# Kernel tuning notes

Measured on AMD Instinct MI355X. Metric: run time of the kernel, lower is better.

The kernel has to match this reference:

```python
import jax, jax.numpy as jnp
import numpy as np

B, T, D, H, G = 256, 1024, 32, 64, 4 * 64  # batch, seq, input, hidden, gates


def setup_inputs() -> dict:
    key = jax.random.key(0)
    ks = jax.random.split(key, 12)
    s = 1.0 / np.sqrt(H)  # PyTorch LSTM default init scale
    return {
        "x": jax.random.normal(ks[0], (B, T, D), dtype=jnp.float32),
        "w_ih_l0": jax.random.normal(ks[1], (G, D), dtype=jnp.float32) * s,
        "w_hh_l0": jax.random.normal(ks[2], (G, H), dtype=jnp.float32) * s,
        "b_ih_l0": jax.random.normal(ks[3], (G,), dtype=jnp.float32) * s,
        "b_hh_l0": jax.random.normal(ks[4], (G,), dtype=jnp.float32) * s,
        "w_ih_l1": jax.random.normal(ks[5], (G, H), dtype=jnp.float32) * s,
        "w_hh_l1": jax.random.normal(ks[6], (G, H), dtype=jnp.float32) * s,
        "b_ih_l1": jax.random.normal(ks[7], (G,), dtype=jnp.float32) * s,
        "b_hh_l1": jax.random.normal(ks[8], (G,), dtype=jnp.float32) * s,
        "w_fc": jax.random.normal(ks[9], (1, H), dtype=jnp.float32) * s,
        "b_fc": jax.random.normal(ks[10], (1,), dtype=jnp.float32) * s,
    }


def _lstm_layer(x, w_ih, w_hh, b_ih, b_hh):
    """x: [B, T, Din] -> h_seq [B, T, H]. PyTorch gate order (i, f, g, o)."""
    # Precompute input contribution for all timesteps in one GEMM.
    gx = jnp.einsum('btd,gd->btg', x, w_ih) + b_ih + b_hh  # [B, T, 4H]
    gx = jnp.swapaxes(gx, 0, 1)  # [T, B, 4H] for scan over time
    h0 = jnp.zeros((x.shape[0], H), dtype=x.dtype)
    c0 = jnp.zeros((x.shape[0], H), dtype=x.dtype)

    def step(carry, g_t):
        h, c = carry
        g = g_t + h @ w_hh.T  # [B, 4H]
        i, f, gg, o = jnp.split(g, 4, axis=-1)
        i = jax.nn.sigmoid(i)
        f = jax.nn.sigmoid(f)
        gg = jnp.tanh(gg)
        o = jax.nn.sigmoid(o)
        c = f * c + i * gg
        h = o * jnp.tanh(c)
        return (h, c), h

    _, h_seq = jax.lax.scan(step, (h0, c0), gx)  # h_seq: [T, B, H]
    return jnp.swapaxes(h_seq, 0, 1)  # [B, T, H]


def reference(x, w_ih_l0, w_hh_l0, b_ih_l0, b_hh_l0,
              w_ih_l1, w_hh_l1, b_ih_l1, b_hh_l1, w_fc, b_fc):
    h1 = _lstm_layer(x, w_ih_l0, w_hh_l0, b_ih_l0, b_hh_l0)
    h2 = _lstm_layer(h1, w_ih_l1, w_hh_l1, b_ih_l1, b_hh_l1)
    last = h2[:, -1, :]  # [B, H]
    logits = last @ w_fc.T + b_fc  # [B, 1]
    return jax.nn.sigmoid(logits)
```

## Files before the change

kernel.cpp:

```cpp
#include <hip/hip_runtime.h>

#define TT 1024
#define DD 32
#define HH 64

typedef __fp16 h2v __attribute__((ext_vector_type(2)));
typedef _Float16 f16x8 __attribute__((ext_vector_type(8)));
typedef float f32x4 __attribute__((ext_vector_type(4)));

struct __attribute__((aligned(16))) H4 { h2v p[4]; };

__device__ __forceinline__ h2v pk(float a, float b) {
    return __builtin_amdgcn_cvt_pkrtz(a, b);
}
__device__ __forceinline__ float fsig(float x) {
    float e = __builtin_amdgcn_exp2f(-1.4426950408889634f * x);
    return __builtin_amdgcn_rcpf(1.0f + e);
}
__device__ __forceinline__ float ftanh(float x) {
    float e = __builtin_amdgcn_exp2f(2.885390081777927f * x);
    return 1.0f - 2.0f * __builtin_amdgcn_rcpf(1.0f + e);
}
__device__ __forceinline__ void bar_lds() {
    asm volatile("s_waitcnt lgkmcnt(0)\n\ts_barrier" ::: "memory");
}
__device__ __forceinline__ float pick4(f32x4 c, bool s0, bool s1) {
    float lo = s0 ? c[1] : c[0];
    float hi = s0 ? c[3] : c[2];
    return s1 ? hi : lo;
}
__device__ __forceinline__ f16x8 load_afrag(const float* p) {
    float4 f0 = *(const float4*)p;
    float4 f1 = *(const float4*)(p + 4);
    H4 t;
    t.p[0] = pk(f0.x, f0.y); t.p[1] = pk(f0.z, f0.w);
    t.p[2] = pk(f1.x, f1.y); t.p[3] = pk(f1.z, f1.w);
    return __builtin_bit_cast(f16x8, t);
}
#define MFMA16(A, B, C) __builtin_amdgcn_mfma_f32_16x16x32_f16(A, B, C, 0, 0, 0)

__global__ __launch_bounds__(512) void lstm2_b4v3(
    const float* __restrict__ x,
    const float* __restrict__ w_ih_l0, const float* __restrict__ w_hh_l0,
    const float* __restrict__ b_ih_l0, const float* __restrict__ b_hh_l0,
    const float* __restrict__ w_ih_l1, const float* __restrict__ w_hh_l1,
    const float* __restrict__ b_ih_l1, const float* __restrict__ b_hh_l1,
    const float* __restrict__ w_fc,   const float* __restrict__ b_fc,
    float* __restrict__ out)
{
    const int bbase = blockIdx.x * 4;
    const int tid  = threadIdx.x;
    const int wave = tid >> 6;
    const int lane = tid & 63;
    const bool isL1 = wave < 4;
    const int js   = wave & 3;
    const int quad = lane >> 4;
    const int bb   = lane & 3;
    const int rsel = (lane >> 2) & 3;
    const int jj   = js*16 + quad*4 + rsel;
    const int mrow = lane & 15;

    __shared__ __attribute__((aligned(16))) __fp16 buf[1280];

    {
        int* bi = (int*)buf;
        bi[tid] = 0;
        if (tid < 128) bi[512 + tid] = 0;
    }

    f16x8 A[16];
    float bs0, bs1, bs2, bs3;
    if (isL1) {
        #pragma unroll
        for (int q = 0; q < 4; ++q) {
            const int g = q*64 + js*16 + mrow;
            A[q*3 + 0] = load_afrag(w_ih_l0 + (size_t)g*DD + quad*8);
            A[q*3 + 1] = load_afrag(w_hh_l0 + (size_t)g*HH + quad*8);
            A[q*3 + 2] = load_afrag(w_hh_l0 + (size_t)g*HH + 32 + quad*8);
        }
        bs0 = b_ih_l0[0*64 + jj] + b_hh_l0[0*64 + jj];
        bs1 = b_ih_l0[1*64 + jj] + b_hh_l0[1*64 + jj];
        bs2 = b_ih_l0[2*64 + jj] + b_hh_l0[2*64 + jj];
        bs3 = b_ih_l0[3*64 + jj] + b_hh_l0[3*64 + jj];
    } else {
        #pragma unroll
        for (int q = 0; q < 4; ++q) {
            const int g = q*64 + js*16 + mrow;
            A[q*4 + 0] = load_afrag(w_ih_l1 + (size_t)g*HH + quad*8);
            A[q*4 + 1] = load_afrag(w_ih_l1 + (size_t)g*HH + 32 + quad*8);
            A[q*4 + 2] = load_afrag(w_hh_l1 + (size_t)g*HH + quad*8);
            A[q*4 + 3] = load_afrag(w_hh_l1 + (size_t)g*HH + 32 + quad*8);
        }
        bs0 = b_ih_l1[0*64 + jj] + b_hh_l1[0*64 + jj];
        bs1 = b_ih_l1[1*64 + jj] + b_hh_l1[1*64 + jj];
        bs2 = b_ih_l1[2*64 + jj] + b_hh_l1[2*64 + jj];
        bs3 = b_ih_l1[3*64 + jj] + b_hh_l1[3*64 + jj];
    }

    const int roff = (bb*4 + quad)*8;
    const int cw   = (isL1 ? 1 : 3) + (jj >> 5);
    const int woff = ((cw*4 + bb)*4 + ((jj & 31) >> 3))*8 + (jj & 7);

    const float* xg = x + (size_t)(bbase + (lane >> 4)) * (TT*DD) + (lane & 15)*2;
    const int sdw = ((lane >> 4)*4 + ((lane & 15) >> 2))*4 + ((lane & 15) & 3);
    float2 xv1 = {0.f, 0.f}, xv2 = {0.f, 0.f};

    __syncthreads();
    if (wave == 7) {
        float2 v0 = *(const float2*)xg;
        ((int*)buf)[sdw] = __builtin_bit_cast(int, pk(v0.x, v0.y));
        xv1 = *(const float2*)(xg + DD);
        xv2 = *(const float2*)(xg + 2*DD);
    }
    __syncthreads();

    const bool s0 = (rsel & 1) != 0;
    const bool s1 = (rsel & 2) != 0;
    float cst = 0.0f;

    for (int t = 0; t <= TT; ++t) {
        const int p = t & 1;
        const __fp16* bc = buf + p*640;
        __fp16* bn = buf + (p ^ 1)*640;
        if (isL1) {
            if (t < TT) {
                f16x8 B0 = *(const f16x8*)(bc + 0*128 + roff);
                f16x8 B1 = *(const f16x8*)(bc + 1*128 + roff);
                f16x8 B2 = *(const f16x8*)(bc + 2*128 + roff);

                f32x4 Z = {0.f, 0.f, 0.f, 0.f};
                f32x4 C0 = Z, C1 = Z, C2 = Z, C3 = Z;
                C0 = MFMA16(A[0], B0, C0); C0 = MFMA16(A[1],  B1, C0); C0 = MFMA16(A[2],  B2, C0);
                C1 = MFMA16(A[3], B0, C1); C1 = MFMA16(A[4],  B1, C1); C1 = MFMA16(A[5],  B2, C1);
                C2 = MFMA16(A[6], B0, C2); C2 = MFMA16(A[7],  B1, C2); C2 = MFMA16(A[8],  B2, C2);
                C3 = MFMA16(A[9], B0, C3); C3 = MFMA16(A[10], B1, C3); C3 = MFMA16(A[11], B2, C3);

                float Si = pick4(C0, s0, s1) + bs0;
                float Sf = pick4(C1, s0, s1) + bs1;
                float Sg = pick4(C2, s0, s1) + bs2;
                float So = pick4(C3, s0, s1) + bs3;

                float ii = fsig(Si), ff = fsig(Sf), oo = fsig(So);
                float gg = ftanh(Sg);
                cst = ff * cst + ii * gg;
                float hv = oo * ftanh(cst);
                bn[woff] = (__fp16)hv;
            }
        } else {
            if (wave == 7 && t < TT) {
                ((int*)bn)[sdw] = __builtin_bit_cast(int, pk(xv1.x, xv1.y));
                xv1 = xv2;
                const int tl = (t + 3 < TT) ? (t + 3) : (TT - 1);
                xv2 = *(const float2*)(xg + (size_t)tl*DD);
            }
            if (t > 0) {
                f16x8 B1 = *(const f16x8*)(bc + 1*128 + roff);
                f16x8 B2 = *(const f16x8*)(bc + 2*128 + roff);
                f16x8 B3 = *(const f16x8*)(bc + 3*128 + roff);
                f16x8 B4 = *(const f16x8*)(bc + 4*128 + roff);

                f32x4 Z = {0.f, 0.f, 0.f, 0.f};
                f32x4 C0 = Z, C1 = Z, C2 = Z, C3 = Z;
                C0 = MFMA16(A[0],  B1, C0); C0 = MFMA16(A[1],  B2, C0);
                C0 = MFMA16(A[2],  B3, C0); C0 = MFMA16(A[3],  B4, C0);
                C1 = MFMA16(A[4],  B1, C1); C1 = MFMA16(A[5],  B2, C1);
                C1 = MFMA16(A[6],  B3, C1); C1 = MFMA16(A[7],  B4, C1);
                C2 = MFMA16(A[8],  B1, C2); C2 = MFMA16(A[9],  B2, C2);
                C2 = MFMA16(A[10], B3, C2); C2 = MFMA16(A[11], B4, C2);
                C3 = MFMA16(A[12], B1, C3); C3 = MFMA16(A[13], B2, C3);
                C3 = MFMA16(A[14], B3, C3); C3 = MFMA16(A[15], B4, C3);

                float Si = pick4(C0, s0, s1) + bs0;
                float Sf = pick4(C1, s0, s1) + bs1;
                float Sg = pick4(C2, s0, s1) + bs2;
                float So = pick4(C3, s0, s1) + bs3;

                float ii = fsig(Si), ff = fsig(Sf), oo = fsig(So);
                float gg = ftanh(Sg);
                cst = ff * cst + ii * gg;
                float hv = oo * ftanh(cst);
                bn[woff] = (__fp16)hv;
            }
        }
        bar_lds();
    }

    if (wave == 0) {
        const int jg = lane >> 2;
        float s = 0.f;
        #pragma unroll
        for (int u2 = 0; u2 < 4; ++u2) {
            const int j = jg*4 + u2;
            float hval = (float)buf[640 + (((3 + (j >> 5))*4 + bb)*4 + ((j & 31) >> 3))*8 + (j & 7)];
            s += hval * w_fc[j];
        }
        s += __shfl_xor(s, 4);
        s += __shfl_xor(s, 8);
        s += __shfl_xor(s, 16);
        s += __shfl_xor(s, 32);
        if (lane < 4) out[bbase + lane] = fsig(s + b_fc[0]);
    }
}

extern "C" void kernel_launch(void* const* d_in, const int* in_sizes, int n_in,
                              void* d_out, int out_size, void* d_ws, size_t ws_size,
                              hipStream_t stream) {
    lstm2_b4v3<<<dim3(64), dim3(512), 0, stream>>>(
        (const float*)d_in[0],
        (const float*)d_in[1], (const float*)d_in[2],
        (const float*)d_in[3], (const float*)d_in[4],
        (const float*)d_in[5], (const float*)d_in[6],
        (const float*)d_in[7], (const float*)d_in[8],
        (const float*)d_in[9], (const float*)d_in[10],
        (float*)d_out);
}
```

Measured before the change: 551.3 us.

## Merge both LSTM layers into each wave, halving block size to four waves

Each wave now computes both layer-0 and layer-1 gates for its 16 hidden units instead of splitting layers across separate wave groups, so the block shrinks from 8 to 4 waves. The shared B1/B2 fragments (layer-0 h) are loaded once and reused by both layers' MFMAs. The aim is a cheaper per-step barrier across fewer waves and less duplicated LDS traffic. The cost is twice the MFMA and transcendental work per wave on the serial critical path, plus more registers held for weights.

```diff
diff --git a/kernel.cpp b/kernel.cpp
--- a/kernel.cpp
+++ b/kernel.cpp
@@ -39,7 +39,7 @@
 }
 #define MFMA16(A, B, C) __builtin_amdgcn_mfma_f32_16x16x32_f16(A, B, C, 0, 0, 0)
 
-__global__ __launch_bounds__(512) void lstm2_b4v3(
+__global__ __launch_bounds__(256) void lstm2_m4(
     const float* __restrict__ x,
     const float* __restrict__ w_ih_l0, const float* __restrict__ w_hh_l0,
     const float* __restrict__ b_ih_l0, const float* __restrict__ b_hh_l0,
@@ -52,8 +52,7 @@
     const int tid  = threadIdx.x;
     const int wave = tid >> 6;
     const int lane = tid & 63;
-    const bool isL1 = wave < 4;
-    const int js   = wave & 3;
+    const int js   = wave;
     const int quad = lane >> 4;
     const int bb   = lane & 3;
     const int rsel = (lane >> 2) & 3;
@@ -61,52 +60,44 @@
     const int mrow = lane & 15;
 
     __shared__ __attribute__((aligned(16))) __fp16 buf[1280];
-
     {
         int* bi = (int*)buf;
-        bi[tid] = 0;
+        bi[tid] = 0; bi[256 + tid] = 0;
         if (tid < 128) bi[512 + tid] = 0;
     }
 
-    f16x8 A[16];
-    float bs0, bs1, bs2, bs3;
-    if (isL1) {
-        #pragma unroll
-        for (int q = 0; q < 4; ++q) {
-            const int g = q*64 + js*16 + mrow;
-            A[q*3 + 0] = load_afrag(w_ih_l0 + (size_t)g*DD + quad*8);
-            A[q*3 + 1] = load_afrag(w_hh_l0 + (size_t)g*HH + quad*8);
-            A[q*3 + 2] = load_afrag(w_hh_l0 + (size_t)g*HH + 32 + quad*8);
-        }
-        bs0 = b_ih_l0[0*64 + jj] + b_hh_l0[0*64 + jj];
-        bs1 = b_ih_l0[1*64 + jj] + b_hh_l0[1*64 + jj];
-        bs2 = b_ih_l0[2*64 + jj] + b_hh_l0[2*64 + jj];
-        bs3 = b_ih_l0[3*64 + jj] + b_hh_l0[3*64 + jj];
-    } else {
-        #pragma unroll
-        for (int q = 0; q < 4; ++q) {
-            const int g = q*64 + js*16 + mrow;
-            A[q*4 + 0] = load_afrag(w_ih_l1 + (size_t)g*HH + quad*8);
-            A[q*4 + 1] = load_afrag(w_ih_l1 + (size_t)g*HH + 32 + quad*8);
-            A[q*4 + 2] = load_afrag(w_hh_l1 + (size_t)g*HH + quad*8);
-            A[q*4 + 3] = load_afrag(w_hh_l1 + (size_t)g*HH + 32 + quad*8);
-        }
-        bs0 = b_ih_l1[0*64 + jj] + b_hh_l1[0*64 + jj];
-        bs1 = b_ih_l1[1*64 + jj] + b_hh_l1[1*64 + jj];
-        bs2 = b_ih_l1[2*64 + jj] + b_hh_l1[2*64 + jj];
-        bs3 = b_ih_l1[3*64 + jj] + b_hh_l1[3*64 + jj];
-    }
-
-    const int roff = (bb*4 + quad)*8;
-    const int cw   = (isL1 ? 1 : 3) + (jj >> 5);
-    const int woff = ((cw*4 + bb)*4 + ((jj & 31) >> 3))*8 + (jj & 7);
+    f16x8 A1[12], A2[16];
+    float b10, b11, b12, b13, b20, b21, b22, b23;
+    #pragma unroll
+    for (int q = 0; q < 4; ++q) {
+        const int g = q*64 + js*16 + mrow;
+        A1[q*3 + 0] = load_afrag(w_ih_l0 + (size_t)g*DD + quad*8);
+        A1[q*3 + 1] = load_afrag(w_hh_l0 + (size_t)g*HH + quad*8);
+        A1[q*3 + 2] = load_afrag(w_hh_l0 + (size_t)g*HH + 32 + quad*8);
+        A2[q*4 + 0] = load_afrag(w_ih_l1 + (size_t)g*HH + quad*8);
+        A2[q*4 + 1] = load_afrag(w_ih_l1 + (size_t)g*HH + 32 + quad*8);
+        A2[q*4 + 2] = load_afrag(w_hh_l1 + (size_t)g*HH + quad*8);
+        A2[q*4 + 3] = load_afrag(w_hh_l1 + (size_t)g*HH + 32 + quad*8);
+    }
+    b10 = b_ih_l0[0*64 + jj] + b_hh_l0[0*64 + jj];
+    b11 = b_ih_l0[1*64 + jj] + b_hh_l0[1*64 + jj];
+    b12 = b_ih_l0[2*64 + jj] + b_hh_l0[2*64 + jj];
+    b13 = b_ih_l0[3*64 + jj] + b_hh_l0[3*64 + jj];
+    b20 = b_ih_l1[0*64 + jj] + b_hh_l1[0*64 + jj];
+    b21 = b_ih_l1[1*64 + jj] + b_hh_l1[1*64 + jj];
+    b22 = b_ih_l1[2*64 + jj] + b_hh_l1[2*64 + jj];
+    b23 = b_ih_l1[3*64 + jj] + b_hh_l1[3*64 + jj];
+
+    const int roff  = (bb*4 + quad)*8;
+    const int woff1 = (((1 + (jj >> 5))*4 + bb)*4 + ((jj & 31) >> 3))*8 + (jj & 7);
+    const int woff2 = (((3 + (jj >> 5))*4 + bb)*4 + ((jj & 31) >> 3))*8 + (jj & 7);
 
     const float* xg = x + (size_t)(bbase + (lane >> 4)) * (TT*DD) + (lane & 15)*2;
     const int sdw = ((lane >> 4)*4 + ((lane & 15) >> 2))*4 + ((lane & 15) & 3);
     float2 xv1 = {0.f, 0.f}, xv2 = {0.f, 0.f};
 
     __syncthreads();
-    if (wave == 7) {
+    if (wave == 3) {
         float2 v0 = *(const float2*)xg;
         ((int*)buf)[sdw] = __builtin_bit_cast(int, pk(v0.x, v0.y));
         xv1 = *(const float2*)(xg + DD);
@@ -116,72 +107,69 @@
 
     const bool s0 = (rsel & 1) != 0;
     const bool s1 = (rsel & 2) != 0;
-    float cst = 0.0f;
+    float c1 = 0.0f, c2 = 0.0f;
+    const f32x4 Z = {0.f, 0.f, 0.f, 0.f};
 
     for (int t = 0; t <= TT; ++t) {
         const int p = t & 1;
         const __fp16* bc = buf + p*640;
         __fp16* bn = buf + (p ^ 1)*640;
-        if (isL1) {
-            if (t < TT) {
-                f16x8 B0 = *(const f16x8*)(bc + 0*128 + roff);
-                f16x8 B1 = *(const f16x8*)(bc + 1*128 + roff);
-                f16x8 B2 = *(const f16x8*)(bc + 2*128 + roff);
-
-                f32x4 Z = {0.f, 0.f, 0.f, 0.f};
-                f32x4 C0 = Z, C1 = Z, C2 = Z, C3 = Z;
-                C0 = MFMA16(A[0], B0, C0); C0 = MFMA16(A[1],  B1, C0); C0 = MFMA16(A[2],  B2, C0);
-                C1 = MFMA16(A[3], B0, C1); C1 = MFMA16(A[4],  B1, C1); C1 = MFMA16(A[5],  B2, C1);
-                C2 = MFMA16(A[6], B0, C2); C2 = MFMA16(A[7],  B1, C2); C2 = MFMA16(A[8],  B2, C2);
-                C3 = MFMA16(A[9], B0, C3); C3 = MFMA16(A[10], B1, C3); C3 = MFMA16(A[11], B2, C3);
-
-                float Si = pick4(C0, s0, s1) + bs0;
-                float Sf = pick4(C1, s0, s1) + bs1;
-                float Sg = pick4(C2, s0, s1) + bs2;
-                float So = pick4(C3, s0, s1) + bs3;
-
-                float ii = fsig(Si), ff = fsig(Sf), oo = fsig(So);
-                float gg = ftanh(Sg);
-                cst = ff * cst + ii * gg;
-                float hv = oo * ftanh(cst);
-                bn[woff] = (__fp16)hv;
-            }
-        } else {
-            if (wave == 7 && t < TT) {
-                ((int*)bn)[sdw] = __builtin_bit_cast(int, pk(xv1.x, xv1.y));
-                xv1 = xv2;
-                const int tl = (t + 3 < TT) ? (t + 3) : (TT - 1);
-                xv2 = *(const float2*)(xg + (size_t)tl*DD);
-            }
-            if (t > 0) {
-                f16x8 B1 = *(const f16x8*)(bc + 1*128 + roff);
-                f16x8 B2 = *(const f16x8*)(bc + 2*128 + roff);
-                f16x8 B3 = *(const f16x8*)(bc + 3*128 + roff);
-                f16x8 B4 = *(const f16x8*)(bc + 4*128 + roff);
-
-                f32x4 Z = {0.f, 0.f, 0.f, 0.f};
-                f32x4 C0 = Z, C1 = Z, C2 = Z, C3 = Z;
-                C0 = MFMA16(A[0],  B1, C0); C0 = MFMA16(A[1],  B2, C0);
-                C0 = MFMA16(A[2],  B3, C0); C0 = MFMA16(A[3],  B4, C0);
-                C1 = MFMA16(A[4],  B1, C1); C1 = MFMA16(A[5],  B2, C1);
-                C1 = MFMA16(A[6],  B3, C1); C1 = MFMA16(A[7],  B4, C1);
-                C2 = MFMA16(A[8],  B1, C2); C2 = MFMA16(A[9],  B2, C2);
-                C2 = MFMA16(A[10], B3, C2); C2 = MFMA16(A[11], B4, C2);
-                C3 = MFMA16(A[12], B1, C3); C3 = MFMA16(A[13], B2, C3);
-                C3 = MFMA16(A[14], B3, C3); C3 = MFMA16(A[15], B4, C3);
-
-                float Si = pick4(C0, s0, s1) + bs0;
-                float Sf = pick4(C1, s0, s1) + bs1;
-                float Sg = pick4(C2, s0, s1) + bs2;
-                float So = pick4(C3, s0, s1) + bs3;
-
-                float ii = fsig(Si), ff = fsig(Sf), oo = fsig(So);
-                float gg = ftanh(Sg);
-                cst = ff * cst + ii * gg;
-                float hv = oo * ftanh(cst);
-                bn[woff] = (__fp16)hv;
-            }
-        }
+
+        f16x8 B1 = *(const f16x8*)(bc + 1*128 + roff);
+        f16x8 B2 = *(const f16x8*)(bc + 2*128 + roff);
+
+        if (wave == 3 && t < TT) {
+            ((int*)bn)[sdw] = __builtin_bit_cast(int, pk(xv1.x, xv1.y));
+            xv1 = xv2;
+            const int tl = (t + 3 < TT) ? (t + 3) : (TT - 1);
+            xv2 = *(const float2*)(xg + (size_t)tl*DD);
+        }
+
+        if (t < TT) {
+            f16x8 B0 = *(const f16x8*)(bc + 0*128 + roff);
+            f32x4 C0 = Z, C1f = Z, C2f = Z, C3f = Z;
+            C0  = MFMA16(A1[0], B0, C0);  C0  = MFMA16(A1[1],  B1, C0);  C0  = MFMA16(A1[2],  B2, C0);
+            C1f = MFMA16(A1[3], B0, C1f); C1f = MFMA16(A1[4],  B1, C1f); C1f = MFMA16(A1[5],  B2, C1f);
+            C2f = MFMA16(A1[6], B0, C2f); C2f = MFMA16(A1[7],  B1, C2f); C2f = MFMA16(A1[8],  B2, C2f);
+            C3f = MFMA16(A1[9], B0, C3f); C3f = MFMA16(A1[10], B1, C3f); C3f = MFMA16(A1[11], B2, C3f);
+
+            float Si = pick4(C0,  s0, s1) + b10;
+            float Sf = pick4(C1f, s0, s1) + b11;
+            float Sg = pick4(C2f, s0, s1) + b12;
+            float So = pick4(C3f, s0, s1) + b13;
+
+            float ii = fsig(Si), ff = fsig(Sf), oo = fsig(So);
+            float gg = ftanh(Sg);
+            c1 = ff * c1 + ii * gg;
+            float hv = oo * ftanh(c1);
+            bn[woff1] = (__fp16)hv;
+        }
+
+        if (t > 0) {
+            f16x8 B3 = *(const f16x8*)(bc + 3*128 + roff);
+            f16x8 B4 = *(const f16x8*)(bc + 4*128 + roff);
+            f32x4 D0 = Z, D1 = Z, D2 = Z, D3 = Z;
+            D0 = MFMA16(A2[0],  B1, D0); D0 = MFMA16(A2[1],  B2, D0);
+            D0 = MFMA16(A2[2],  B3, D0); D0 = MFMA16(A2[3],  B4, D0);
+            D1 = MFMA16(A2[4],  B1, D1); D1 = MFMA16(A2[5],  B2, D1);
+            D1 = MFMA16(A2[6],  B3, D1); D1 = MFMA16(A2[7],  B4, D1);
+            D2 = MFMA16(A2[8],  B1, D2); D2 = MFMA16(A2[9],  B2, D2);
+            D2 = MFMA16(A2[10], B3, D2); D2 = MFMA16(A2[11], B4, D2);
+            D3 = MFMA16(A2[12], B1, D3); D3 = MFMA16(A2[13], B2, D3);
+            D3 = MFMA16(A2[14], B3, D3); D3 = MFMA16(A2[15], B4, D3);
+
+            float Si = pick4(D0, s0, s1) + b20;
+            float Sf = pick4(D1, s0, s1) + b21;
+            float Sg = pick4(D2, s0, s1) + b22;
+            float So = pick4(D3, s0, s1) + b23;
+
+            float ii = fsig(Si), ff = fsig(Sf), oo = fsig(So);
+            float gg = ftanh(Sg);
+            c2 = ff * c2 + ii * gg;
+            float hv = oo * ftanh(c2);
+            bn[woff2] = (__fp16)hv;
+        }
+
         bar_lds();
     }
 
@@ -205,7 +193,7 @@
 extern "C" void kernel_launch(void* const* d_in, const int* in_sizes, int n_in,
                               void* d_out, int out_size, void* d_ws, size_t ws_size,
                               hipStream_t stream) {
-    lstm2_b4v3<<<dim3(64), dim3(512), 0, stream>>>(
+    lstm2_m4<<<dim3(64), dim3(256), 0, stream>>>(
         (const float*)d_in[0],
         (const float*)d_in[1], (const float*)d_in[2],
         (const float*)d_in[3], (const float*)d_in[4],
```

Measured after the change: 885.3 us. 1.61x slower.
